# Kernel tuning notes

Measured on AMD Instinct MI355X. Metric: run time of the kernel, lower is better.

The kernel has to match this reference:

```python
import jax, jax.numpy as jnp
import numpy as np

DIM = 512
HEADS = 8
DIM_HEAD = 64
INNER = HEADS * DIM_HEAD  # 512
NARROW_K = 9
WIDE_K = 9
WIDE_DIL = 5


def setup_inputs() -> dict:
    key = jax.random.key(0)
    ks = jax.random.split(key, 12)
    b, n = 4, 2048
    s = lambda fan_in: 1.0 / np.sqrt(fan_in)
    inp = {
        'tokens': jax.random.normal(ks[0], (b, n, DIM), jnp.float32),
        'mask': jax.random.randint(ks[1], (b, n), 0, 2) > 0,
        'w_qkv': jax.random.normal(ks[2], (DIM, INNER * 3), jnp.float32) * s(DIM),
        'w_out': jax.random.normal(ks[3], (INNER, DIM), jnp.float32) * s(INNER),
        'b_out': jnp.zeros((DIM,), jnp.float32),
        'w_narrow': jax.random.normal(ks[4], (DIM, DIM, NARROW_K), jnp.float32) * s(DIM * NARROW_K),
        'b_narrow': jnp.zeros((DIM,), jnp.float32),
        'w_wide': jax.random.normal(ks[5], (DIM, DIM, WIDE_K), jnp.float32) * s(DIM * WIDE_K),
        'b_wide': jnp.zeros((DIM,), jnp.float32),
        'ln1_g': jnp.ones((DIM,), jnp.float32),
        'ln1_b': jnp.zeros((DIM,), jnp.float32),
        'ff_w': jax.random.normal(ks[6], (DIM, DIM), jnp.float32) * s(DIM),
        'ff_b': jnp.zeros((DIM,), jnp.float32),
        'ln2_g': jnp.ones((DIM,), jnp.float32),
        'ln2_b': jnp.zeros((DIM,), jnp.float32),
    }
    return inp


def layer_norm(x, g, b, eps=1e-5):
    m = jnp.mean(x, axis=-1, keepdims=True)
    v = jnp.mean(jnp.square(x - m), axis=-1, keepdims=True)
    return (x - m) / jnp.sqrt(v + eps) * g + b


def rope_encoding(seq_len, dim_head, dtype):
    inv_freq = 1.0 / (10000.0 ** (jnp.arange(0, dim_head, 2, dtype=jnp.float32) / dim_head))
    pos = jnp.arange(seq_len, dtype=jnp.float32)
    sinu = jnp.einsum('i,j->ij', pos, inv_freq)  # [n, d/2]
    return jnp.concatenate([jnp.sin(sinu), jnp.cos(sinu)], axis=-1).astype(dtype)  # [n, d]


def attn(tokens, mask, w_qkv, w_out, b_out):
    b, n, _ = tokens.shape
    qkv = tokens @ w_qkv  # [b, n, 3*inner]
    q, k, v = jnp.split(qkv, 3, axis=-1)
    reshp = lambda t: t.reshape(b, n, HEADS, DIM_HEAD).transpose(0, 2, 1, 3)  # b h n d
    q, k, v = reshp(q), reshp(k), reshp(v)
    rope = rope_encoding(n, DIM_HEAD, tokens.dtype)  # [n, d]
    q = q + rope
    k = k + rope
    mask4 = mask[:, None, :, None]  # b 1 n 1
    big = jnp.finfo(k.dtype).max
    k = jnp.where(mask4, k, -big)
    q = jax.nn.softmax(q, axis=-1) * (DIM_HEAD ** -0.5)
    k = jax.nn.softmax(k, axis=2)  # over n
    v = jnp.where(mask4, v, 0.0)
    context = jnp.einsum('bhnd,bhne->bhde', k, v)
    out = jnp.einsum('bhde,bhnd->bhne', context, q)
    out = out.transpose(0, 2, 1, 3).reshape(b, n, INNER)
    return out @ w_out + b_out


def conv1d(x, w, b, padding, dilation):
    # x: [b, c, n], w: [out, in, k]
    y = jax.lax.conv_general_dilated(
        x, w, window_strides=(1,), padding=[(padding, padding)],
        rhs_dilation=(dilation,), dimension_numbers=('NCW', 'OIW', 'NCW'))
    return y + b[None, :, None]


def reference(tokens, mask, w_qkv, w_out, b_out, w_narrow, b_narrow,
              w_wide, b_wide, ln1_g, ln1_b, ff_w, ff_b, ln2_g, ln2_b):
    tokens = attn(tokens, mask, w_qkv, w_out, b_out)
    conv_in = tokens.transpose(0, 2, 1)  # b d n
    conv_in = jnp.where(mask[:, None, :], conv_in, 0.0)
    narrow = jax.nn.gelu(conv1d(conv_in, w_narrow, b_narrow, NARROW_K // 2, 1), approximate=False)
    wide_pad = (WIDE_K + (WIDE_K - 1) * (WIDE_DIL - 1)) // 2  # 20
    wide = jax.nn.gelu(conv1d(conv_in, w_wide, b_wide, wide_pad, WIDE_DIL), approximate=False)
    tokens = tokens + narrow.transpose(0, 2, 1) + wide.transpose(0, 2, 1)
    tokens = layer_norm(tokens, ln1_g, ln1_b)
    tokens = layer_norm(jax.nn.gelu(tokens @ ff_w + ff_b, approximate=False), ln2_g, ln2_b)
    return tokens
```

## Files before the change

### kernel.cpp

```cpp
#include <hip/hip_runtime.h>
#include <hip/hip_bf16.h>

#define BB 4
#define NN 2048
#define NROWS (BB*NN)

typedef unsigned short u16;
typedef __bf16 bf16x8 __attribute__((ext_vector_type(8)));
typedef u16    u16x8  __attribute__((ext_vector_type(8)));
typedef u16    u16x2  __attribute__((ext_vector_type(2)));
typedef float  fx4    __attribute__((ext_vector_type(4)));

__device__ __forceinline__ float bf2f(u16 u){
  union { float f; unsigned int i; } x; x.i = ((unsigned int)u) << 16; return x.f;
}
__device__ __forceinline__ u16 f2bf(float f){
  union { float f; unsigned int i; } x; x.f = f;
  unsigned int i = x.i;
  i += 0x7fffu + ((i >> 16) & 1u);
  return (u16)(i >> 16);
}
__device__ __forceinline__ float geluf(float x){
  return 0.5f * x * (1.0f + erff(x * 0.70710678118654752f));
}
__device__ __forceinline__ void gload16(const void* g, void* l){
  __builtin_amdgcn_global_load_lds((const __attribute__((address_space(1))) unsigned int*)g,
                                   (__attribute__((address_space(3))) unsigned int*)l, 16, 0, 0);
}

__global__ __launch_bounds__(256) void sniff_k(const u16* tokens, const unsigned int* mask, int* flags){
  __shared__ int s_f32, s_byte;
  if (threadIdx.x == 0) { s_f32 = 0; s_byte = 0; }
  __syncthreads();
  for (int i = threadIdx.x; i < 4096; i += 256) {
    float v = bf2f(tokens[i]);
    if (!(fabsf(v) < 1e10f)) atomicOr(&s_f32, 1);
  }
  for (int i = threadIdx.x; i < 2048; i += 256) {
    if (mask[i] > 1u) atomicOr(&s_byte, 1);
  }
  __syncthreads();
  if (threadIdx.x == 0) { flags[0] = s_f32; flags[1] = s_byte; }
}

__global__ __launch_bounds__(256) void misc2_k(const void* mask, const void* tokens,
                                               const void* p0, const void* p1, const void* p2,
                                               const void* p3, const void* p4, const void* p5,
                                               const void* p6, const void* p7,
                                               const int* flags, float* rope, int* m32,
                                               float* params, float* ctx, float* kS, u16* tokbf,
                                               const void* w_qkv, const void* w_out, const void* ff_w,
                                               const void* w_narrow, const void* w_wide,
                                               u16* wqkvt, u16* woutt, u16* ffwt,
                                               u16* wtN2, u16* wtW2){
  int bid = blockIdx.x;
  int tid = threadIdx.x;
  int f = flags[0];
  if (bid < 8192) {
    const void* srcs[8] = {p0,p1,p2,p3,p4,p5,p6,p7};
    int mbyte = flags[1];
    const int T = 131072 + 8192 + 4096 + 131072 + 2048 + 4194304;
    for (int i = bid*256 + tid; i < T; i += 8192*256) {
      if (i < 131072) {
        int p = i >> 6, j = i & 63;
        int jj = (j < 32) ? j : j - 32;
        float invf = exp2f(-(float)jj * (13.287712379549449f/32.0f));
        float prod = (float)p * invf;
        rope[i] = (j < 32) ? sinf(prod) : cosf(prod);
      } else if (i < 139264) {
        int k = i - 131072;
        int v = mbyte ? (int)((const unsigned char*)mask)[k] : ((const int*)mask)[k];
        m32[k] = v ? 1 : 0;
      } else if (i < 143360) {
        int k = i - 139264;
        int pid = k >> 9, j = k & 511;
        const void* s = srcs[pid];
        params[k] = f ? ((const float*)s)[j] : bf2f(((const u16*)s)[j]);
      } else if (i < 274432) {
        ctx[i - 143360] = 0.0f;
      } else if (i < 276480) {
        kS[i - 274432] = 0.0f;
      } else {
        int k = i - 276480;
        tokbf[k] = f ? f2bf(((const float*)tokens)[k]) : ((const u16*)tokens)[k];
      }
    }
  } else if (bid < 9216) {
    int id = bid - 8192;
    int tensor = id >> 9, o = id & 511;
    const void* src = tensor ? w_wide : w_narrow;
    u16* dst = tensor ? wtW2 : wtN2;
    __shared__ u16 Ls[4608];
    for (int i = tid; i < 4608; i += 256) {
      Ls[i] = f ? f2bf(((const float*)src)[(size_t)o*4608 + i]) : ((const u16*)src)[(size_t)o*4608 + i];
    }
    __syncthreads();
    #pragma unroll
    for (int kk = 0; kk < 9; kk++) {
      #pragma unroll
      for (int u = 0; u < 2; u++) {
        int c = tid + u*256;
        dst[(size_t)kk*262144 + o*512 + c] = Ls[c*9 + kk];
      }
    }
  } else {
    int id = bid - 9216;
    int z = id / 192;
    int rem = id - z*192;
    int x = rem % 24, y = rem / 24;
    int Nn = (z == 0) ? 1536 : 512;
    if (x * 64 >= Nn) return;
    const void* src = (z == 0) ? w_qkv : (z == 1) ? w_out : ff_w;
    u16* dst = (z == 0) ? wqkvt : (z == 1) ? woutt : ffwt;
    __shared__ u16 Ts[64][72];
    int n0 = x * 64, k0 = y * 64;
    int r = tid >> 2, cq = (tid & 3) * 16;
    #pragma unroll
    for (int u = 0; u < 2; u++) {
      int c = cq + u*8;
      int sidx = (k0 + r)*Nn + n0 + c;
      u16x8 v;
      if (f) {
        #pragma unroll
        for (int j = 0; j < 8; j++) v[j] = f2bf(((const float*)src)[sidx + j]);
      } else {
        v = *(const u16x8*)&((const u16*)src)[sidx];
      }
      *(u16x8*)&Ts[r][c] = v;
    }
    __syncthreads();
    #pragma unroll
    for (int u = 0; u < 2; u++) {
      int c = cq + u*8;
      u16x8 v;
      #pragma unroll
      for (int j = 0; j < 8; j++) v[j] = Ts[c + j][r];
      *(u16x8*)&dst[(size_t)(n0 + r)*512 + k0 + c] = v;
    }
  }
}

__global__ __launch_bounds__(256) void mgemm_qkv_k(const u16* A, const u16* Bt, const float* rope,
                                                   const int* mask, u16* qb, u16* keb, u16* vb){
  __shared__ u16 As[128*32];
  __shared__ u16 Bs[128*32];
  __shared__ int smask[128];
  int tid = threadIdx.x;
  int lane = tid & 63;
  int wave = tid >> 6;
  int wm = (wave >> 1) * 64, wn = (wave & 1) * 64;
  int quad = lane >> 4, l16 = lane & 15;
  int m0 = blockIdx.y * 128, n0 = blockIdx.x * 128;
  fx4 acc[4][4] = {};
  for (int k0 = 0; k0 < 512; k0 += 32) {
    #pragma unroll
    for (int it = 0; it < 2; it++) {
      int s = it*256 + tid;
      int lsl = ((s & 3) ^ ((s >> 3) & 3)) * 8;
      gload16(&A[(size_t)(m0 + (s >> 2))*512 + k0 + lsl], &As[(it*256 + wave*64)*8]);
    }
    #pragma unroll
    for (int it = 0; it < 2; it++) {
      int s = it*256 + tid;
      int lsl = ((s & 3) ^ ((s >> 3) & 3)) * 8;
      gload16(&Bt[(size_t)(n0 + (s >> 2))*512 + k0 + lsl], &Bs[(it*256 + wave*64)*8]);
    }
    __syncthreads();
    bf16x8 af[4], bfv[4];
    #pragma unroll
    for (int i = 0; i < 4; i++) {
      int row = wm + i*16 + l16;
      af[i] = __builtin_bit_cast(bf16x8,
                *(const u16x8*)&As[row*32 + ((quad ^ ((row >> 1) & 3)) * 8)]);
    }
    #pragma unroll
    for (int j = 0; j < 4; j++) {
      int row = wn + j*16 + l16;
      bfv[j] = __builtin_bit_cast(bf16x8,
                *(const u16x8*)&Bs[row*32 + ((quad ^ ((row >> 1) & 3)) * 8)]);
    }
    #pragma unroll
    for (int i = 0; i < 4; i++)
      #pragma unroll
      for (int j = 0; j < 4; j++)
        acc[i][j] = __builtin_amdgcn_mfma_f32_16x16x32_bf16(af[i], bfv[j], acc[i][j], 0, 0, 0);
    __syncthreads();
  }
  int x = blockIdx.x;
  if (x >= 4) {
    if (tid < 128) smask[tid] = mask[m0 + tid];
    __syncthreads();
  }
  if (x < 4) {
    #pragma unroll
    for (int i = 0; i < 4; i++)
      #pragma unroll
      for (int r = 0; r < 4; r++) {
        int rl = wm + i*16 + quad*4 + r;
        int row = m0 + rl;
        int nseq = row & (NN-1);
        const float* rp = rope + nseq*64 + l16;
        float e0 = __expf(acc[i][0][r] + rp[0]);
        float e1 = __expf(acc[i][1][r] + rp[16]);
        float e2 = __expf(acc[i][2][r] + rp[32]);
        float e3 = __expf(acc[i][3][r] + rp[48]);
        float s = e0 + e1 + e2 + e3;
        s += __shfl_xor(s, 1); s += __shfl_xor(s, 2);
        s += __shfl_xor(s, 4); s += __shfl_xor(s, 8);
        float sc = 0.125f / s;
        size_t base = (size_t)row*512 + n0 + wn + l16;
        qb[base]      = f2bf(e0*sc);
        qb[base + 16] = f2bf(e1*sc);
        qb[base + 32] = f2bf(e2*sc);
        qb[base + 48] = f2bf(e3*sc);
      }
  } else if (x < 8) {
    #pragma unroll
    for (int i = 0; i < 4; i++)
      #pragma unroll
      for (int r = 0; r < 4; r++) {
        int rl = wm + i*16 + quad*4 + r;
        int row = m0 + rl;
        int nseq = row & (NN-1);
        int mk = smask[rl];
        const float* rp = rope + nseq*64 + l16;
        size_t base = (size_t)row*512 + (n0 - 512) + wn + l16;
        #pragma unroll
        for (int j = 0; j < 4; j++) {
          float ke = mk ? __expf(acc[i][j][r] + rp[j*16]) : 0.0f;
          keb[base + j*16] = f2bf(ke);
        }
      }
  } else {
    #pragma unroll
    for (int i = 0; i < 4; i++)
      #pragma unroll
      for (int r = 0; r < 4; r++) {
        int rl = wm + i*16 + quad*4 + r;
        int row = m0 + rl;
        int mk = smask[rl];
        size_t base = (size_t)row*512 + (n0 - 1024) + wn + l16;
        #pragma unroll
        for (int j = 0; j < 4; j++)
          vb[base + j*16] = mk ? f2bf(acc[i][j][r]) : (u16)0;
      }
  }
}

#define FMA16(a, b, acc) \
  acc[0][0] = fmaf(a.x, b.x, acc[0][0]); acc[0][1] = fmaf(a.x, b.y, acc[0][1]); \
  acc[0][2] = fmaf(a.x, b.z, acc[0][2]); acc[0][3] = fmaf(a.x, b.w, acc[0][3]); \
  acc[1][0] = fmaf(a.y, b.x, acc[1][0]); acc[1][1] = fmaf(a.y, b.y, acc[1][1]); \
  acc[1][2] = fmaf(a.y, b.z, acc[1][2]); acc[1][3] = fmaf(a.y, b.w, acc[1][3]); \
  acc[2][0] = fmaf(a.z, b.x, acc[2][0]); acc[2][1] = fmaf(a.z, b.y, acc[2][1]); \
  acc[2][2] = fmaf(a.z, b.z, acc[2][2]); acc[2][3] = fmaf(a.z, b.w, acc[2][3]); \
  acc[3][0] = fmaf(a.w, b.x, acc[3][0]); acc[3][1] = fmaf(a.w, b.y, acc[3][1]); \
  acc[3][2] = fmaf(a.w, b.z, acc[3][2]); acc[3][3] = fmaf(a.w, b.w, acc[3][3]);

__global__ __launch_bounds__(256) void ctx_k(const u16* keb, const u16* vb, float* ctx, float* Sg){
  int bh = blockIdx.x, seg = blockIdx.y;
  int b = bh >> 3, h = bh & 7;
  __shared__ float Ks[32][68], Vs[32][68];
  __shared__ float sS[64];
  int tid = threadIdx.x, tx = tid & 15, ty = tid >> 4;
  if (tid < 64) sS[tid] = 0.0f;
  float acc[4][4] = {{0.f,0.f,0.f,0.f},{0.f,0.f,0.f,0.f},{0.f,0.f,0.f,0.f},{0.f,0.f,0.f,0.f}};
  float sp[8] = {0,0,0,0,0,0,0,0};
  int nl = tid >> 3, dcol = (tid & 7)*8;
  const u16* kp0 = keb + (size_t)(b*NN + seg*256)*512 + h*64 + dcol;
  const u16* vp0 = vb  + (size_t)(b*NN + seg*256)*512 + h*64 + dcol;
  for (int nc = 0; nc < 256; nc += 32) {
    u16x8 ku = *(const u16x8*)(kp0 + (size_t)(nc + nl)*512);
    u16x8 vu = *(const u16x8*)(vp0 + (size_t)(nc + nl)*512);
    float a[8], bb[8];
    #pragma unroll
    for (int t = 0; t < 8; t++) { a[t] = bf2f(ku[t]); bb[t] = bf2f(vu[t]); sp[t] += a[t]; }
    *(float4*)&Ks[nl][dcol]   = (float4){a[0],a[1],a[2],a[3]};
    *(float4*)&Ks[nl][dcol+4] = (float4){a[4],a[5],a[6],a[7]};
    *(float4*)&Vs[nl][dcol]   = (float4){bb[0],bb[1],bb[2],bb[3]};
    *(float4*)&Vs[nl][dcol+4] = (float4){bb[4],bb[5],bb[6],bb[7]};
    __syncthreads();
    #pragma unroll
    for (int q = 0; q < 32; q++) {
      float4 a4 = *(const float4*)&Ks[q][ty*4];
      float4 b4 = *(const float4*)&Vs[q][tx*4];
      FMA16(a4, b4, acc)
    }
    __syncthreads();
  }
  #pragma unroll
  for (int j = 0; j < 8; j++) atomicAdd(&sS[dcol + j], sp[j]);
  float* cp = ctx + (size_t)bh*4096;
  #pragma unroll
  for (int i = 0; i < 4; i++)
    #pragma unroll
    for (int j = 0; j < 4; j++)
      atomicAdd(&cp[(ty*4 + i)*64 + tx*4 + j], acc[i][j]);
  __syncthreads();
  if (tid < 64) atomicAdd(&Sg[bh*64 + tid], sS[tid]);
}

__global__ __launch_bounds__(256) void ctxw_k(const float* ctx, const float* Sg, const u16* woutt,
                                              u16* W2t, u16* cpadb){
  int bx = blockIdx.x;
  int tid = threadIdx.x;
  if (bx >= 32) {
    int idx = (bx - 32)*256 + tid;
    if (idx < BB*40*512) {
      int c = idx & 511;
      int t = (idx >> 9) % 40;
      int b = idx / (40*512);
      int tt = (t < 20) ? t : 2048 + t;
      cpadb[((size_t)b*2088 + tt)*512 + c] = 0;
    }
    return;
  }
  int h = bx & 7, b = bx >> 3;
  int lane = tid & 63, wave = tid >> 6;
  int quad = lane >> 4, l16 = lane & 15;
  const float* cp = ctx + (size_t)(b*8 + h)*4096;
  fx4 acc[8][4] = {};
  #pragma unroll
  for (int ks = 0; ks < 2; ks++) {
    bf16x8 bfv[4];
    #pragma unroll
    for (int j = 0; j < 4; j++) {
      int d = j*16 + l16;
      float S = Sg[(b*8 + h)*64 + d];
      float rs = (S > 0.0f) ? 1.0f/S : 0.0f;
      const float* src = cp + d*64 + ks*32 + quad*8;
      float4 v0 = *(const float4*)src, v1 = *(const float4*)(src + 4);
      bf16x8 t;
      t[0]=(__bf16)(v0.x*rs); t[1]=(__bf16)(v0.y*rs); t[2]=(__bf16)(v0.z*rs); t[3]=(__bf16)(v0.w*rs);
      t[4]=(__bf16)(v1.x*rs); t[5]=(__bf16)(v1.y*rs); t[6]=(__bf16)(v1.z*rs); t[7]=(__bf16)(v1.w*rs);
      bfv[j] = t;
    }
    #pragma unroll
    for (int i = 0; i < 8; i++) {
      int orow = wave*128 + i*16 + l16;
      bf16x8 afr = __builtin_bit_cast(bf16x8, *(const u16x8*)&woutt[(size_t)orow*512 + h*64 + ks*32 + quad*8]);
      #pragma unroll
      for (int j = 0; j < 4; j++)
        acc[i][j] = __builtin_amdgcn_mfma_f32_16x16x32_bf16(afr, bfv[j], acc[i][j], 0, 0, 0);
    }
  }
  u16* out = W2t + (size_t)b*262144;
  #pragma unroll
  for (int i = 0; i < 8; i++)
    #pragma unroll
    for (int j = 0; j < 4; j++)
      #pragma unroll
      for (int r = 0; r < 4; r++) {
        int orow = wave*128 + i*16 + quad*4 + r;
        out[(size_t)orow*512 + h*64 + j*16 + l16] = f2bf(acc[i][j][r]);
      }
}

__global__ __launch_bounds__(256) void mgemm_attn64_k(const u16* qb, const u16* W2t, const float* bias,
                                                      const int* mask, u16* attnb, u16* cpadb){
  __shared__ u16 As[64][40];
  __shared__ u16 Bs[128][40];
  int tid = threadIdx.x;
  int lane = tid & 63;
  int wave = tid >> 6;
  int wn = wave * 32;
  int quad = lane >> 4, l16 = lane & 15;
  int m0 = blockIdx.y * 64, n0 = blockIdx.x * 128, b = blockIdx.z;
  const u16* A  = qb  + (size_t)b*2048*512;
  const u16* Bt = W2t + (size_t)b*262144;
  fx4 acc[4][2] = {};
  int ar = tid >> 2;
  int ac = (tid & 3) * 8;
  for (int k0 = 0; k0 < 512; k0 += 32) {
    *(u16x8*)&As[ar][ac]    = *(const u16x8*)&A[(size_t)(m0+ar)*512 + k0 + ac];
    *(u16x8*)&Bs[ar][ac]    = *(const u16x8*)&Bt[(size_t)(n0+ar)*512 + k0 + ac];
    *(u16x8*)&Bs[ar+64][ac] = *(const u16x8*)&Bt[(size_t)(n0+ar+64)*512 + k0 + ac];
    __syncthreads();
    bf16x8 af[4], bfv[2];
    #pragma unroll
    for (int i = 0; i < 4; i++)
      af[i] = __builtin_bit_cast(bf16x8, *(const u16x8*)&As[i*16 + l16][quad*8]);
    #pragma unroll
    for (int j = 0; j < 2; j++)
      bfv[j] = __builtin_bit_cast(bf16x8, *(const u16x8*)&Bs[wn + j*16 + l16][quad*8]);
    #pragma unroll
    for (int i = 0; i < 4; i++)
      #pragma unroll
      for (int j = 0; j < 2; j++)
        acc[i][j] = __builtin_amdgcn_mfma_f32_16x16x32_bf16(af[i], bfv[j], acc[i][j], 0, 0, 0);
    __syncthreads();
  }
  #pragma unroll
  for (int i = 0; i < 4; i++)
    #pragma unroll
    for (int j = 0; j < 2; j++) {
      int col = n0 + wn + j*16 + l16;
      float bv = bias[col];
      #pragma unroll
      for (int r = 0; r < 4; r++) {
        int row_l = m0 + i*16 + quad*4 + r;
        float v = acc[i][j][r] + bv;
        u16 vbb = f2bf(v);
        attnb[((size_t)b*2048 + row_l)*512 + col] = vbb;
        int mk = mask[b*2048 + row_l];
        cpadb[((size_t)b*2088 + row_l + 20)*512 + col] = mk ? vbb : (u16)0;
      }
    }
}

#define A_ROWS 552
#define A_SZ (A_ROWS*32)
#define W_SZ (9*64*32)
__global__ __launch_bounds__(512, 2) void mconv15_k(const u16* cpad, const u16* Wn, const u16* Ww,
                                                    const float* bias_n, const float* bias_w,
                                                    u16* Dn, u16* Dw){
  __shared__ u16 As[2*A_SZ];
  __shared__ u16 Ws[2*W_SZ];
  int tid = threadIdx.x;
  int lane = tid & 63;
  int wave = tid >> 6;
  int wm = wave * 64;
  int quad = lane >> 4, l16 = lane & 15;
  int o0 = blockIdx.x * 64, m0 = blockIdx.y * 512;
  int b = blockIdx.z >> 1, cid = blockIdx.z & 1;
  const u16* W = cid ? Ww : Wn;
  const float* bias = cid ? bias_w : bias_n;
  u16* D = cid ? Dw : Dn;
  fx4 acc[4][4] = {};
  const u16* cb = cpad + ((size_t)b*2088 + m0)*512;
  int wslot = ((quad ^ ((l16 >> 1) & 3)) * 8);
  int sbase = cid ? 0 : 16;
  int sstep = cid ? 5 : 1;
  int rowb0 = sbase + wm + l16;

  const u16* ap[5]; bool av[5];
  #pragma unroll
  for (int it = 0; it < 5; it++) {
    int s = it*512 + tid;
    av[it] = (s < 2208);
    int row = av[it] ? (s >> 2) : 0;
    int lsl = ((s & 3) ^ ((s >> 3) & 3)) * 8;
    ap[it] = cb + (size_t)row*512 + lsl;
  }
  const u16* wp[5]; bool wv[5];
  #pragma unroll
  for (int it = 0; it < 5; it++) {
    int s = it*512 + tid;
    wv[it] = (s < 2304);
    int kk = wv[it] ? (s >> 8) : 0;
    int ow = (s >> 2) & 63;
    int lsl = ((s & 3) ^ ((s >> 3) & 3)) * 8;
    wp[it] = W + (size_t)kk*262144 + (size_t)(o0 + ow)*512 + lsl;
  }

#define STAGE_CHUNK(c0, buf)                                                          \
  {                                                                                   \
    _Pragma("unroll")                                                                 \
    for (int it = 0; it < 5; it++) {                                                  \
      if (av[it])                                                                     \
        gload16(ap[it] + (c0), &As[(buf)*A_SZ + (it*512 + wave*64)*8]);               \
    }                                                                                 \
    _Pragma("unroll")                                                                 \
    for (int it = 0; it < 5; it++) {                                                  \
      if (wv[it])                                                                     \
        gload16(wp[it] + (c0), &Ws[(buf)*W_SZ + (it*512 + wave*64)*8]);               \
    }                                                                                 \
  }

#define LOADFRAG(kk, bfv, afr)                                                        \
  {                                                                                   \
    int rowb = rowb0 + sstep*(kk);                                                    \
    int aslot = ((quad ^ ((rowb >> 1) & 3)) * 8);                                     \
    _Pragma("unroll")                                                                 \
    for (int j = 0; j < 4; j++)                                                       \
      bfv[j] = __builtin_bit_cast(bf16x8,                                             \
                 *(const u16x8*)&Wsb[((kk)*64 + j*16 + l16)*32 + wslot]);             \
    _Pragma("unroll")                                                                 \
    for (int i = 0; i < 4; i++)                                                       \
      afr[i] = __builtin_bit_cast(bf16x8,                                             \
                 *(const u16x8*)&Asb[(rowb + i*16)*32 + aslot]);                      \
  }

#define MFMATAP_SGB(bfv, afr)                                                         \
  {                                                                                   \
    _Pragma("unroll")                                                                 \
    for (int i = 0; i < 4; i++)                                                       \
      _Pragma("unroll")                                                               \
      for (int j = 0; j < 4; j++)                                                     \
        acc[i][j] = __builtin_amdgcn_mfma_f32_16x16x32_bf16(afr[i], bfv[j],           \
                                                            acc[i][j], 0, 0, 0);      \
    _Pragma("unroll")                                                                 \
    for (int g = 0; g < 8; g++) {                                                     \
      __builtin_amdgcn_sched_group_barrier(0x008, 2, 0);                  \
      __builtin_amdgcn_sched_group_barrier(0x100, 1, 0);               \
    }                                                                                 \
  }

#define MFMATAP_PLAIN(bfv, afr)                                                       \
  {                                                                                   \
    _Pragma("unroll")                                                                 \
    for (int i = 0; i < 4; i++)                                                       \
      _Pragma("unroll")                                                               \
      for (int j = 0; j < 4; j++)                                                     \
        acc[i][j] = __builtin_amdgcn_mfma_f32_16x16x32_bf16(afr[i], bfv[j],           \
                                                            acc[i][j], 0, 0, 0);      \
  }

  STAGE_CHUNK(0, 0)
  __syncthreads();

  for (int ch = 0; ch < 16; ch++) {
    int cur = ch & 1;
    const u16* Asb = &As[cur*A_SZ];
    const u16* Wsb = &Ws[cur*W_SZ];
    bf16x8 bfvA[4], afrA[4], bfvB[4], afrB[4];
    LOADFRAG(0, bfvA, afrA)
    if (ch < 15) {
      int c0n = (ch + 1) * 32;
      int nb = cur ^ 1;
      STAGE_CHUNK(c0n, nb)
    }
    #pragma unroll
    for (int kt = 0; kt < 8; kt += 2) {
      LOADFRAG(kt+1, bfvB, afrB)
      MFMATAP_SGB(bfvA, afrA)
      LOADFRAG(kt+2, bfvA, afrA)
      MFMATAP_SGB(bfvB, afrB)
    }
    MFMATAP_PLAIN(bfvA, afrA)
    __syncthreads();
  }
#undef STAGE_CHUNK
#undef LOADFRAG
#undef MFMATAP_SGB
#undef MFMATAP_PLAIN
  #pragma unroll
  for (int i = 0; i < 4; i++)
    #pragma unroll
    for (int j = 0; j < 4; j++) {
      int col = o0 + j*16 + l16;
      float bv = bias[col];
      #pragma unroll
      for (int r = 0; r < 4; r++) {
        int row = b*2048 + m0 + wm + i*16 + quad*4 + r;
        D[(size_t)row*512 + col] = f2bf(geluf(acc[i][j][r] + bv));
      }
    }
}

__global__ __launch_bounds__(512) void mgemm128b_k(const u16* A, const u16* Bt, const float* bias,
                                                   u16* C){
  __shared__ u16 As[128*32];
  __shared__ u16 Bs[128*32];
  int tid = threadIdx.x;
  int lane = tid & 63;
  int wave = tid >> 6;
  int wm = (wave >> 2) * 64;
  int wn = (wave & 3) * 32;
  int quad = lane >> 4, l16 = lane & 15;
  int m0 = blockIdx.y * 128, n0 = blockIdx.x * 128;
  fx4 acc[4][2] = {};
  for (int k0 = 0; k0 < 512; k0 += 32) {
    {
      int s = tid;
      int lsl = ((s & 3) ^ ((s >> 3) & 3)) * 8;
      gload16(&A[(size_t)(m0 + (s >> 2))*512 + k0 + lsl], &As[(wave*64)*8]);
    }
    {
      int s = tid;
      int lsl = ((s & 3) ^ ((s >> 3) & 3)) * 8;
      gload16(&Bt[(size_t)(n0 + (s >> 2))*512 + k0 + lsl], &Bs[(wave*64)*8]);
    }
    __syncthreads();
    bf16x8 af[4], bfv[2];
    #pragma unroll
    for (int i = 0; i < 4; i++) {
      int row = wm + i*16 + l16;
      af[i] = __builtin_bit_cast(bf16x8,
                *(const u16x8*)&As[row*32 + ((quad ^ ((row >> 1) & 3)) * 8)]);
    }
    #pragma unroll
    for (int j = 0; j < 2; j++) {
      int row = wn + j*16 + l16;
      bfv[j] = __builtin_bit_cast(bf16x8,
                *(const u16x8*)&Bs[row*32 + ((quad ^ ((row >> 1) & 3)) * 8)]);
    }
    #pragma unroll
    for (int i = 0; i < 4; i++)
      #pragma unroll
      for (int j = 0; j < 2; j++)
        acc[i][j] = __builtin_amdgcn_mfma_f32_16x16x32_bf16(af[i], bfv[j], acc[i][j], 0, 0, 0);
    __syncthreads();
  }
  #pragma unroll
  for (int i = 0; i < 4; i++)
    #pragma unroll
    for (int j = 0; j < 2; j++) {
      int col = n0 + wn + j*16 + l16;
      float bv = bias[col];
      #pragma unroll
      for (int r = 0; r < 4; r++) {
        int row = m0 + wm + i*16 + quad*4 + r;
        C[(size_t)row*512 + col] = f2bf(geluf(acc[i][j][r] + bv));
      }
    }
}

__device__ __forceinline__ float block_sum512(float v, float* red){
  #pragma unroll
  for (int o = 32; o; o >>= 1) v += __shfl_xor(v, o, 64);
  int w = threadIdx.x >> 6;
  if ((threadIdx.x & 63) == 0) red[w] = v;
  __syncthreads();
  float t = red[0] + red[1] + red[2] + red[3];
  __syncthreads();
  return t;
}

template<int NADD, int OM>
__global__ __launch_bounds__(256) void ln_k(const u16* X, const u16* Y, const u16* Z,
                                            const float* g, const float* be,
                                            const int* flags, void* out){
  __shared__ float red[4];
  size_t row = blockIdx.x;
  int tid = threadIdx.x;
  int c = tid * 2;
  u16x2 xv = *(const u16x2*)&X[row*512 + c];
  float x0 = bf2f(xv[0]), x1 = bf2f(xv[1]);
  if (NADD >= 1) { u16x2 yv = *(const u16x2*)&Y[row*512 + c]; x0 += bf2f(yv[0]); x1 += bf2f(yv[1]); }
  if (NADD >= 2) { u16x2 zv = *(const u16x2*)&Z[row*512 + c]; x0 += bf2f(zv[0]); x1 += bf2f(zv[1]); }
  float mean = block_sum512(x0 + x1, red) * (1.0f/512.0f);
  float d0 = x0 - mean, d1 = x1 - mean;
  float var = block_sum512(d0*d0 + d1*d1, red) * (1.0f/512.0f);
  float inv = rsqrtf(var + 1e-5f);
  float2 gv = *(const float2*)&g[c];
  float2 bv = *(const float2*)&be[c];
  float r0 = d0*inv*gv.x + bv.x;
  float r1 = d1*inv*gv.y + bv.y;
  bool obf = (OM == 1) || (OM == 2 && !flags[0]);
  if (obf) {
    u16x2 ov; ov[0] = f2bf(r0); ov[1] = f2bf(r1);
    *(u16x2*)&((u16*)out)[row*512 + c] = ov;
  } else {
    float2 ov; ov.x = r0; ov.y = r1;
    *(float2*)&((float*)out)[row*512 + c] = ov;
  }
}

extern "C" void kernel_launch(void* const* d_in, const int* in_sizes, int n_in,
                              void* d_out, int out_size, void* d_ws, size_t ws_size,
                              hipStream_t stream) {
  const void* tokens   = d_in[0];
  const void* mask     = d_in[1];
  const void* w_qkv    = d_in[2];
  const void* w_out    = d_in[3];
  const void* b_out    = d_in[4];
  const void* w_narrow = d_in[5];
  const void* b_narrow = d_in[6];
  const void* w_wide   = d_in[7];
  const void* b_wide   = d_in[8];
  const void* ln1_g    = d_in[9];
  const void* ln1_b    = d_in[10];
  const void* ff_w     = d_in[11];
  const void* ff_b     = d_in[12];
  const void* ln2_g    = d_in[13];
  const void* ln2_b    = d_in[14];

  float* ws = (float*)d_ws;
  int*   flags  = (int*)ws;
  int*   m32    = (int*)(ws + 16);
  float* params = ws + 8208;
  float* kS     = ws + 12304;
  float* ctx    = ws + 14352;
  float* rope   = ws + 145424;
  u16*   tokbf  = (u16*)(ws + 276496);
  u16*   wqkvt  = (u16*)(ws + 2373648);
  u16*   woutt  = (u16*)(ws + 2766864);
  u16*   ffwt   = (u16*)(ws + 2897936);
  u16*   wtN2   = (u16*)(ws + 3029008);
  u16*   wtW2   = (u16*)(ws + 4208656);
  u16*   qb     = (u16*)(ws + 5388304);
  u16*   keb    = (u16*)(ws + 7485456);
  u16*   vb     = (u16*)(ws + 9582608);
  u16*   W2t    = (u16*)(ws + 11679760);
  u16*   attnb  = (u16*)(ws + 12204048);
  u16*   cpadb  = (u16*)(ws + 14301200);
  u16*   Dnb    = (u16*)(ws + 16439312);
  u16*   Dwb    = (u16*)(ws + 18536464);
  u16*   Eb     = attnb;
  u16*   t1b    = tokbf;

  float* p_bout = params;        float* p_bnar = params + 512;
  float* p_bwid = params + 1024; float* p_l1g  = params + 1536;
  float* p_l1b  = params + 2048; float* p_ffb  = params + 2560;
  float* p_l2g  = params + 3072; float* p_l2b  = params + 3584;

  sniff_k<<<dim3(1), dim3(256), 0, stream>>>((const u16*)tokens, (const unsigned int*)mask, flags);

  misc2_k<<<dim3(9792), dim3(256), 0, stream>>>(mask, tokens, b_out, b_narrow, b_wide, ln1_g, ln1_b,
                                                ff_b, ln2_g, ln2_b, flags, rope, m32, params, ctx,
                                                kS, tokbf, w_qkv, w_out, ff_w, w_narrow, w_wide,
                                                wqkvt, woutt, ffwt, wtN2, wtW2);

  mgemm_qkv_k<<<dim3(12, 64), dim3(256), 0, stream>>>(
      tokbf, wqkvt, rope, m32, qb, keb, vb);

  ctx_k<<<dim3(32, 8), dim3(256), 0, stream>>>(keb, vb, ctx, kS);

  ctxw_k<<<dim3(352), dim3(256), 0, stream>>>(ctx, kS, woutt, W2t, cpadb);

  mgemm_attn64_k<<<dim3(4, 32, 4), dim3(256), 0, stream>>>(qb, W2t, p_bout, m32, attnb, cpadb);

  mconv15_k<<<dim3(8, 4, 8), dim3(512), 0, stream>>>(cpadb, wtN2, wtW2, p_bnar, p_bwid, Dnb, Dwb);

  ln_k<2,1><<<dim3(NROWS), dim3(256), 0, stream>>>(attnb, Dnb, Dwb, p_l1g, p_l1b, flags, (void*)t1b);

  mgemm128b_k<<<dim3(4, 64), dim3(512), 0, stream>>>(t1b, ffwt, p_ffb, Eb);

  ln_k<0,2><<<dim3(NROWS), dim3(256), 0, stream>>>(Eb, nullptr, nullptr, p_l2g, p_l2b, flags, d_out);
}
```

Before: 321.9 us.

## Trim misc prep, split ctx partials without atomics, wave-per-row layernorm

Several independent changes land together. The misc kernel stops zeroing ctx and kS and skips the token bf16 copy when inputs are already bf16, letting the QKV GEMM read raw tokens directly; the fp32 path now converts with vector loads. ctx_k uses 16 sequence segments that write plain partial results to scratch (reusing the Dnb/Dwb buffers) instead of atomics, and ctxw_k sums the 16 partials. LayerNorm now handles one row per wave with 8-wide vector loads and shuffle-only reductions, so block syncs go away; the cost is that ctxw_k reads 16x more ctx data.

```diff
diff --git a/kernel.cpp b/kernel.cpp
--- a/kernel.cpp
+++ b/kernel.cpp
@@ -8,7 +8,7 @@
 typedef unsigned short u16;
 typedef __bf16 bf16x8 __attribute__((ext_vector_type(8)));
 typedef u16    u16x8  __attribute__((ext_vector_type(8)));
-typedef u16    u16x2  __attribute__((ext_vector_type(2)));
+typedef u16    u16x4  __attribute__((ext_vector_type(4)));
 typedef float  fx4    __attribute__((ext_vector_type(4)));
 
 __device__ __forceinline__ float bf2f(u16 u){
@@ -48,7 +48,7 @@
                                                const void* p3, const void* p4, const void* p5,
                                                const void* p6, const void* p7,
                                                const int* flags, float* rope, int* m32,
-                                               float* params, float* ctx, float* kS, u16* tokbf,
+                                               float* params, u16* tokbf,
                                                const void* w_qkv, const void* w_out, const void* ff_w,
                                                const void* w_narrow, const void* w_wide,
                                                u16* wqkvt, u16* woutt, u16* ffwt,
@@ -56,11 +56,11 @@
   int bid = blockIdx.x;
   int tid = threadIdx.x;
   int f = flags[0];
-  if (bid < 8192) {
+  if (bid < 2048) {
     const void* srcs[8] = {p0,p1,p2,p3,p4,p5,p6,p7};
     int mbyte = flags[1];
-    const int T = 131072 + 8192 + 4096 + 131072 + 2048 + 4194304;
-    for (int i = bid*256 + tid; i < T; i += 8192*256) {
+    const int T = 131072 + 8192 + 4096 + 1048576;
+    for (int i = bid*256 + tid; i < T; i += 2048*256) {
       if (i < 131072) {
         int p = i >> 6, j = i & 63;
         int jj = (j < 32) ? j : j - 32;
@@ -76,17 +76,16 @@
         int pid = k >> 9, j = k & 511;
         const void* s = srcs[pid];
         params[k] = f ? ((const float*)s)[j] : bf2f(((const u16*)s)[j]);
-      } else if (i < 274432) {
-        ctx[i - 143360] = 0.0f;
-      } else if (i < 276480) {
-        kS[i - 274432] = 0.0f;
-      } else {
-        int k = i - 276480;
-        tokbf[k] = f ? f2bf(((const float*)tokens)[k]) : ((const u16*)tokens)[k];
-      }
-    }
-  } else if (bid < 9216) {
-    int id = bid - 8192;
+      } else if (f) {
+        int k4 = (i - 143360) * 4;
+        float4 v = *(const float4*)&((const float*)tokens)[k4];
+        u16x4 o;
+        o[0] = f2bf(v.x); o[1] = f2bf(v.y); o[2] = f2bf(v.z); o[3] = f2bf(v.w);
+        *(u16x4*)&tokbf[k4] = o;
+      }
+    }
+  } else if (bid < 3072) {
+    int id = bid - 2048;
     int tensor = id >> 9, o = id & 511;
     const void* src = tensor ? w_wide : w_narrow;
     u16* dst = tensor ? wtW2 : wtN2;
@@ -104,7 +103,7 @@
       }
     }
   } else {
-    int id = bid - 9216;
+    int id = bid - 3072;
     int z = id / 192;
     int rem = id - z*192;
     int x = rem % 24, y = rem / 24;
@@ -140,8 +139,10 @@
   }
 }
 
-__global__ __launch_bounds__(256) void mgemm_qkv_k(const u16* A, const u16* Bt, const float* rope,
-                                                   const int* mask, u16* qb, u16* keb, u16* vb){
+__global__ __launch_bounds__(256) void mgemm_qkv_k(const void* tok_raw, const u16* tokbf,
+                                                   const u16* Bt, const float* rope,
+                                                   const int* mask, const int* flags,
+                                                   u16* qb, u16* keb, u16* vb){
   __shared__ u16 As[128*32];
   __shared__ u16 Bs[128*32];
   __shared__ int smask[128];
@@ -151,6 +152,7 @@
   int wm = (wave >> 1) * 64, wn = (wave & 1) * 64;
   int quad = lane >> 4, l16 = lane & 15;
   int m0 = blockIdx.y * 128, n0 = blockIdx.x * 128;
+  const u16* A = flags[0] ? tokbf : (const u16*)tok_raw;
   fx4 acc[4][4] = {};
   for (int k0 = 0; k0 < 512; k0 += 32) {
     #pragma unroll
@@ -257,7 +259,7 @@
   acc[3][0] = fmaf(a.w, b.x, acc[3][0]); acc[3][1] = fmaf(a.w, b.y, acc[3][1]); \
   acc[3][2] = fmaf(a.w, b.z, acc[3][2]); acc[3][3] = fmaf(a.w, b.w, acc[3][3]);
 
-__global__ __launch_bounds__(256) void ctx_k(const u16* keb, const u16* vb, float* ctx, float* Sg){
+__global__ __launch_bounds__(256) void ctx_k(const u16* keb, const u16* vb, float* ctxp, float* Sgp){
   int bh = blockIdx.x, seg = blockIdx.y;
   int b = bh >> 3, h = bh & 7;
   __shared__ float Ks[32][68], Vs[32][68];
@@ -267,9 +269,9 @@
   float acc[4][4] = {{0.f,0.f,0.f,0.f},{0.f,0.f,0.f,0.f},{0.f,0.f,0.f,0.f},{0.f,0.f,0.f,0.f}};
   float sp[8] = {0,0,0,0,0,0,0,0};
   int nl = tid >> 3, dcol = (tid & 7)*8;
-  const u16* kp0 = keb + (size_t)(b*NN + seg*256)*512 + h*64 + dcol;
-  const u16* vp0 = vb  + (size_t)(b*NN + seg*256)*512 + h*64 + dcol;
-  for (int nc = 0; nc < 256; nc += 32) {
+  const u16* kp0 = keb + (size_t)(b*NN + seg*128)*512 + h*64 + dcol;
+  const u16* vp0 = vb  + (size_t)(b*NN + seg*128)*512 + h*64 + dcol;
+  for (int nc = 0; nc < 128; nc += 32) {
     u16x8 ku = *(const u16x8*)(kp0 + (size_t)(nc + nl)*512);
     u16x8 vu = *(const u16x8*)(vp0 + (size_t)(nc + nl)*512);
     float a[8], bb[8];
@@ -290,17 +292,17 @@
   }
   #pragma unroll
   for (int j = 0; j < 8; j++) atomicAdd(&sS[dcol + j], sp[j]);
-  float* cp = ctx + (size_t)bh*4096;
+  float* cp = ctxp + ((size_t)seg*32 + bh)*4096;
   #pragma unroll
   for (int i = 0; i < 4; i++)
     #pragma unroll
     for (int j = 0; j < 4; j++)
-      atomicAdd(&cp[(ty*4 + i)*64 + tx*4 + j], acc[i][j]);
+      cp[(ty*4 + i)*64 + tx*4 + j] = acc[i][j];
   __syncthreads();
-  if (tid < 64) atomicAdd(&Sg[bh*64 + tid], sS[tid]);
-}
-
-__global__ __launch_bounds__(256) void ctxw_k(const float* ctx, const float* Sg, const u16* woutt,
+  if (tid < 64) Sgp[(size_t)seg*2048 + bh*64 + tid] = sS[tid];
+}
+
+__global__ __launch_bounds__(256) void ctxw_k(const float* ctxp, const float* Sgp, const u16* woutt,
                                               u16* W2t, u16* cpadb){
   int bx = blockIdx.x;
   int tid = threadIdx.x;
@@ -318,7 +320,16 @@
   int h = bx & 7, b = bx >> 3;
   int lane = tid & 63, wave = tid >> 6;
   int quad = lane >> 4, l16 = lane & 15;
-  const float* cp = ctx + (size_t)(b*8 + h)*4096;
+  int bh = b*8 + h;
+  float rs[4];
+  #pragma unroll
+  for (int j = 0; j < 4; j++) {
+    int d = j*16 + l16;
+    float S = 0.0f;
+    #pragma unroll
+    for (int s = 0; s < 16; s++) S += Sgp[(size_t)s*2048 + bh*64 + d];
+    rs[j] = (S > 0.0f) ? 1.0f/S : 0.0f;
+  }
   fx4 acc[8][4] = {};
   #pragma unroll
   for (int ks = 0; ks < 2; ks++) {
@@ -326,13 +337,17 @@
     #pragma unroll
     for (int j = 0; j < 4; j++) {
       int d = j*16 + l16;
-      float S = Sg[(b*8 + h)*64 + d];
-      float rs = (S > 0.0f) ? 1.0f/S : 0.0f;
-      const float* src = cp + d*64 + ks*32 + quad*8;
-      float4 v0 = *(const float4*)src, v1 = *(const float4*)(src + 4);
+      fx4 v0 = {}, v1 = {};
+      #pragma unroll
+      for (int s = 0; s < 16; s++) {
+        const float* src = ctxp + ((size_t)s*32 + bh)*4096 + d*64 + ks*32 + quad*8;
+        v0 += *(const fx4*)src;
+        v1 += *(const fx4*)(src + 4);
+      }
+      float r = rs[j];
       bf16x8 t;
-      t[0]=(__bf16)(v0.x*rs); t[1]=(__bf16)(v0.y*rs); t[2]=(__bf16)(v0.z*rs); t[3]=(__bf16)(v0.w*rs);
-      t[4]=(__bf16)(v1.x*rs); t[5]=(__bf16)(v1.y*rs); t[6]=(__bf16)(v1.z*rs); t[7]=(__bf16)(v1.w*rs);
+      t[0]=(__bf16)(v0[0]*r); t[1]=(__bf16)(v0[1]*r); t[2]=(__bf16)(v0[2]*r); t[3]=(__bf16)(v0[3]*r);
+      t[4]=(__bf16)(v1[0]*r); t[5]=(__bf16)(v1[1]*r); t[6]=(__bf16)(v1[2]*r); t[7]=(__bf16)(v1[3]*r);
       bfv[j] = t;
     }
     #pragma unroll
@@ -606,44 +621,58 @@
     }
 }
 
-__device__ __forceinline__ float block_sum512(float v, float* red){
-  #pragma unroll
-  for (int o = 32; o; o >>= 1) v += __shfl_xor(v, o, 64);
-  int w = threadIdx.x >> 6;
-  if ((threadIdx.x & 63) == 0) red[w] = v;
-  __syncthreads();
-  float t = red[0] + red[1] + red[2] + red[3];
-  __syncthreads();
-  return t;
-}
-
 template<int NADD, int OM>
-__global__ __launch_bounds__(256) void ln_k(const u16* X, const u16* Y, const u16* Z,
-                                            const float* g, const float* be,
-                                            const int* flags, void* out){
-  __shared__ float red[4];
-  size_t row = blockIdx.x;
-  int tid = threadIdx.x;
-  int c = tid * 2;
-  u16x2 xv = *(const u16x2*)&X[row*512 + c];
-  float x0 = bf2f(xv[0]), x1 = bf2f(xv[1]);
-  if (NADD >= 1) { u16x2 yv = *(const u16x2*)&Y[row*512 + c]; x0 += bf2f(yv[0]); x1 += bf2f(yv[1]); }
-  if (NADD >= 2) { u16x2 zv = *(const u16x2*)&Z[row*512 + c]; x0 += bf2f(zv[0]); x1 += bf2f(zv[1]); }
-  float mean = block_sum512(x0 + x1, red) * (1.0f/512.0f);
-  float d0 = x0 - mean, d1 = x1 - mean;
-  float var = block_sum512(d0*d0 + d1*d1, red) * (1.0f/512.0f);
-  float inv = rsqrtf(var + 1e-5f);
-  float2 gv = *(const float2*)&g[c];
-  float2 bv = *(const float2*)&be[c];
-  float r0 = d0*inv*gv.x + bv.x;
-  float r1 = d1*inv*gv.y + bv.y;
+__global__ __launch_bounds__(256) void lnw_k(const u16* X, const u16* Y, const u16* Z,
+                                             const float* g, const float* be,
+                                             const int* flags, void* out){
+  int wave = threadIdx.x >> 6, lane = threadIdx.x & 63;
+  size_t row = (size_t)blockIdx.x*4 + wave;
+  int c = lane*8;
+  float x[8];
+  {
+    u16x8 xv = *(const u16x8*)&X[row*512 + c];
+    #pragma unroll
+    for (int t = 0; t < 8; t++) x[t] = bf2f(xv[t]);
+  }
+  if (NADD >= 1) {
+    u16x8 yv = *(const u16x8*)&Y[row*512 + c];
+    #pragma unroll
+    for (int t = 0; t < 8; t++) x[t] += bf2f(yv[t]);
+  }
+  if (NADD >= 2) {
+    u16x8 zv = *(const u16x8*)&Z[row*512 + c];
+    #pragma unroll
+    for (int t = 0; t < 8; t++) x[t] += bf2f(zv[t]);
+  }
+  float s = 0.0f;
+  #pragma unroll
+  for (int t = 0; t < 8; t++) s += x[t];
+  #pragma unroll
+  for (int o = 32; o; o >>= 1) s += __shfl_xor(s, o, 64);
+  float mean = s * (1.0f/512.0f);
+  float d[8], s2 = 0.0f;
+  #pragma unroll
+  for (int t = 0; t < 8; t++) { d[t] = x[t] - mean; s2 += d[t]*d[t]; }
+  #pragma unroll
+  for (int o = 32; o; o >>= 1) s2 += __shfl_xor(s2, o, 64);
+  float inv = rsqrtf(s2 * (1.0f/512.0f) + 1e-5f);
+  float4 g0 = *(const float4*)&g[c],  g1 = *(const float4*)&g[c+4];
+  float4 b0 = *(const float4*)&be[c], b1 = *(const float4*)&be[c+4];
+  float r[8];
+  r[0] = d[0]*inv*g0.x + b0.x; r[1] = d[1]*inv*g0.y + b0.y;
+  r[2] = d[2]*inv*g0.z + b0.z; r[3] = d[3]*inv*g0.w + b0.w;
+  r[4] = d[4]*inv*g1.x + b1.x; r[5] = d[5]*inv*g1.y + b1.y;
+  r[6] = d[6]*inv*g1.z + b1.z; r[7] = d[7]*inv*g1.w + b1.w;
   bool obf = (OM == 1) || (OM == 2 && !flags[0]);
   if (obf) {
-    u16x2 ov; ov[0] = f2bf(r0); ov[1] = f2bf(r1);
-    *(u16x2*)&((u16*)out)[row*512 + c] = ov;
+    u16x8 ov;
+    #pragma unroll
+    for (int t = 0; t < 8; t++) ov[t] = f2bf(r[t]);
+    *(u16x8*)&((u16*)out)[row*512 + c] = ov;
   } else {
-    float2 ov; ov.x = r0; ov.y = r1;
-    *(float2*)&((float*)out)[row*512 + c] = ov;
+    float* op = (float*)out + row*512 + c;
+    *(float4*)op       = (float4){r[0], r[1], r[2], r[3]};
+    *(float4*)(op + 4) = (float4){r[4], r[5], r[6], r[7]};
   }
 }
 
@@ -689,6 +718,8 @@
   u16*   Dwb    = (u16*)(ws + 18536464);
   u16*   Eb     = attnb;
   u16*   t1b    = tokbf;
+  float* ctxp   = (float*)Dnb;
+  float* Sgp    = (float*)Dwb;
 
   float* p_bout = params;        float* p_bnar = params + 512;
   float* p_bwid = params + 1024; float* p_l1g  = params + 1536;
@@ -697,25 +728,25 @@
 
   sniff_k<<<dim3(1), dim3(256), 0, stream>>>((const u16*)tokens, (const unsigned int*)mask, flags);
 
-  misc2_k<<<dim3(9792), dim3(256), 0, stream>>>(mask, tokens, b_out, b_narrow, b_wide, ln1_g, ln1_b,
-                                                ff_b, ln2_g, ln2_b, flags, rope, m32, params, ctx,
-                                                kS, tokbf, w_qkv, w_out, ff_w, w_narrow, w_wide,
+  misc2_k<<<dim3(3648), dim3(256), 0, stream>>>(mask, tokens, b_out, b_narrow, b_wide, ln1_g, ln1_b,
+                                                ff_b, ln2_g, ln2_b, flags, rope, m32, params,
+                                                tokbf, w_qkv, w_out, ff_w, w_narrow, w_wide,
                                                 wqkvt, woutt, ffwt, wtN2, wtW2);
 
   mgemm_qkv_k<<<dim3(12, 64), dim3(256), 0, stream>>>(
-      tokbf, wqkvt, rope, m32, qb, keb, vb);
-
-  ctx_k<<<dim3(32, 8), dim3(256), 0, stream>>>(keb, vb, ctx, kS);
-
-  ctxw_k<<<dim3(352), dim3(256), 0, stream>>>(ctx, kS, woutt, W2t, cpadb);
+      tokens, tokbf, wqkvt, rope, m32, flags, qb, keb, vb);
+
+  ctx_k<<<dim3(32, 16), dim3(256), 0, stream>>>(keb, vb, ctxp, Sgp);
+
+  ctxw_k<<<dim3(352), dim3(256), 0, stream>>>(ctxp, Sgp, woutt, W2t, cpadb);
 
   mgemm_attn64_k<<<dim3(4, 32, 4), dim3(256), 0, stream>>>(qb, W2t, p_bout, m32, attnb, cpadb);
 
   mconv15_k<<<dim3(8, 4, 8), dim3(512), 0, stream>>>(cpadb, wtN2, wtW2, p_bnar, p_bwid, Dnb, Dwb);
 
-  ln_k<2,1><<<dim3(NROWS), dim3(256), 0, stream>>>(attnb, Dnb, Dwb, p_l1g, p_l1b, flags, (void*)t1b);
+  lnw_k<2,1><<<dim3(NROWS/4), dim3(256), 0, stream>>>(attnb, Dnb, Dwb, p_l1g, p_l1b, flags, (void*)t1b);
 
   mgemm128b_k<<<dim3(4, 64), dim3(512), 0, stream>>>(t1b, ffwt, p_ffb, Eb);
 
-  ln_k<0,2><<<dim3(NROWS), dim3(256), 0, stream>>>(Eb, nullptr, nullptr, p_l2g, p_l2b, flags, d_out);
-}
+  lnw_k<0,2><<<dim3(NROWS/4), dim3(256), 0, stream>>>(Eb, nullptr, nullptr, p_l2g, p_l2b, flags, d_out);
+}
```

After: 337.7 us. +4.9%, slower.
